# Performance work log

Measured on AMD Instinct MI355X. Metric: run time of the kernel, lower is better.

## Reference

```python
import jax, jax.numpy as jnp
import numpy as np

N_NODES = 100000
N_EDGES = 800000
D_IN = 128
D_HID = 128
N_CLASSES = 64


def _glorot(key, shape):
    fan_in, fan_out = shape[0], shape[1]
    lim = jnp.sqrt(6.0 / (fan_in + fan_out)).astype(jnp.float32)
    return jax.random.uniform(key, shape, jnp.float32, -lim, lim)


def setup_inputs() -> dict:
    key = jax.random.key(0)
    ks = jax.random.split(key, 20)
    inp = {
        "x": jax.random.normal(ks[0], (N_NODES, D_IN), jnp.float32),
        "edge_src": jax.random.randint(ks[1], (N_EDGES,), 0, N_NODES, jnp.int32),
        "edge_dst": jax.random.randint(ks[2], (N_EDGES,), 0, N_NODES, jnp.int32),
    }
    dims = [(D_IN, D_HID), (D_HID, D_HID), (D_HID, N_CLASSES)]
    k = 3
    for i, (di, do) in enumerate(dims):
        inp[f"Wp{i}"] = _glorot(ks[k], (di, di)); k += 1   # fc_pool: d_in -> d_in
        inp[f"bp{i}"] = jnp.zeros((di,), jnp.float32)
        inp[f"Ws{i}"] = _glorot(ks[k], (di, do)); k += 1   # fc_self (no bias)
        inp[f"Wn{i}"] = _glorot(ks[k], (di, do)); k += 1   # fc_neigh
        inp[f"bn{i}"] = jnp.zeros((do,), jnp.float32)
    return inp


def _sage_pool_layer(x, src, dst, Wp, bp, Ws, Wn, bn):
    # pool aggregator: max over in-edges of relu(fc_pool(h_src))
    m = jax.nn.relu(x @ Wp + bp)                 # [N, d_in]
    msg = m[src]                                 # [E, d_in] gather
    agg = jax.ops.segment_max(msg, dst, num_segments=N_NODES)  # scatter-max
    agg = jnp.where(jnp.isfinite(agg), agg, 0.0)  # zero-in-degree nodes -> 0
    return x @ Ws + agg @ Wn + bn


def reference(x, edge_src, edge_dst,
              Wp0, bp0, Ws0, Wn0, bn0,
              Wp1, bp1, Ws1, Wn1, bn1,
              Wp2, bp2, Ws2, Wn2, bn2):
    layers = [
        (Wp0, bp0, Ws0, Wn0, bn0),
        (Wp1, bp1, Ws1, Wn1, bn1),
        (Wp2, bp2, Ws2, Wn2, bn2),
    ]
    h = x
    for (Wp, bp, Ws, Wn, bn) in layers:
        # SAGEConv internal activation=relu followed by wrapper F.relu (idempotent)
        h = jax.nn.relu(_sage_pool_layer(h, edge_src, edge_dst, Wp, bp, Ws, Wn, bn))
    return jax.nn.log_softmax(h, axis=-1)
```

## Files before the change

### kernel.cpp

```cpp
#include <hip/hip_runtime.h>
#include <cstddef>
#include <cstdint>

#define NNODES 100000
#define NEDGES 800000
#define CAP 32
#define NXCD 8
#define NPB (NNODES / NXCD)
#define BINCAP 110592

typedef unsigned short u16;
typedef __attribute__((ext_vector_type(8))) short short8;
typedef __attribute__((ext_vector_type(8))) _Float16 half8;
typedef __attribute__((ext_vector_type(4))) float f32x4;
typedef __attribute__((ext_vector_type(4))) int int4v;

__device__ __forceinline__ u16 f32_to_bf16(float f) {
    union { float f; uint32_t u; } v; v.f = f;
    uint32_t r = v.u + 0x7FFF + ((v.u >> 16) & 1);
    return (u16)(r >> 16);
}
__device__ __forceinline__ u16 f32_to_f16(float f) {
    union { _Float16 h; u16 u; } v; v.h = (_Float16)f;
    return v.u;
}
__device__ __forceinline__ uint32_t pkmax(uint32_t a, uint32_t b) {
    uint32_t lo = max(a & 0xFFFFu, b & 0xFFFFu);
    uint32_t hi = max(a >> 16, b >> 16);
    return lo | (hi << 16);
}

__global__ __launch_bounds__(256) void zero_kernel(float4* __restrict__ p, int n4) {
    int i = blockIdx.x * blockDim.x + threadIdx.x;
    const int stride = gridDim.x * blockDim.x;
    for (; i < n4; i += stride) p[i] = make_float4(0.f, 0.f, 0.f, 0.f);
}

__global__ __launch_bounds__(256) void bin_kernel(
    const int* __restrict__ src, const int* __restrict__ dst,
    int* __restrict__ gcnt, int* __restrict__ bind, int* __restrict__ bins, int E)
{
    __shared__ int ld[1024], ls[1024];
    __shared__ int lcnt[8], lpre[8], lgb[8];
    const int tid = threadIdx.x;
    const int base = blockIdx.x * 1024;

    if (tid < 8) lcnt[tid] = 0;
    __syncthreads();

    int d[4], s[4], slot[4], b[4];
    int nv = 0;
    if (base + tid * 4 + 3 < E) {
        const int4v dd = *(const int4v*)&dst[base + tid * 4];
        const int4v ss = *(const int4v*)&src[base + tid * 4];
#pragma unroll
        for (int j = 0; j < 4; ++j) { d[j] = dd[j]; s[j] = ss[j]; }
        nv = 4;
    } else {
        for (int j = 0; j < 4; ++j) {
            const int idx = base + tid * 4 + j;
            if (idx < E) { d[nv] = dst[idx]; s[nv] = src[idx]; ++nv; }
        }
    }
#pragma unroll 4
    for (int j = 0; j < nv; ++j) {
        b[j] = d[j] / NPB;
        slot[j] = atomicAdd(&lcnt[b[j]], 1);
    }
    __syncthreads();
    if (tid == 0) {
        int run = 0;
#pragma unroll
        for (int k = 0; k < 8; ++k) { lpre[k] = run; run += lcnt[k]; }
    }
    __syncthreads();
#pragma unroll 4
    for (int j = 0; j < nv; ++j) {
        const int p = lpre[b[j]] + slot[j];
        ld[p] = d[j]; ls[p] = s[j];
    }
    if (tid < 8 && lcnt[tid] > 0) lgb[tid] = atomicAdd(&gcnt[tid], lcnt[tid]);
    __syncthreads();
    const int total = lpre[7] + lcnt[7];
    for (int i = tid; i < total; i += 256) {
        const int d_ = ld[i];
        const int b_ = d_ / NPB;
        const int g = lgb[b_] + (i - lpre[b_]);
        if (g < BINCAP) {
            bind[b_ * BINCAP + g] = d_;
            bins[b_ * BINCAP + g] = ls[i];
        }
    }
}

__global__ __launch_bounds__(256) void scatter_fill_kernel(
    const int* __restrict__ gcnt,
    const int* __restrict__ bind, const int* __restrict__ bins,
    int* __restrict__ deg, int* __restrict__ col2)
{
    const int xcd  = blockIdx.x & (NXCD - 1);
    const int grp  = blockIdx.x >> 3;
    const int ngrp = gridDim.x >> 3;
    int cnt = gcnt[xcd]; if (cnt > BINCAP) cnt = BINCAP;
    const int* bd = bind + xcd * BINCAP;
    const int* bs = bins + xcd * BINCAP;
    for (int i = grp * 256 + threadIdx.x; i < cnt; i += ngrp * 256) {
        const int d = bd[i];
        const int r = atomicAdd(&deg[d], 1);
        if (r < CAP) col2[d * CAP + r] = bs[i];
    }
}

struct WPtrs { const float* w[9]; };

__global__ __launch_bounds__(256) void split_weights_kernel(WPtrs p, u16* __restrict__ wbase)
{
    const int idx = blockIdx.x * 256 + threadIdx.x;
    const int w = blockIdx.y;
    const int DO_ = (w >= 7) ? 64 : 128;
    if (idx >= 128 * DO_) return;
    const float v = p.w[w][idx];
    const int k = idx / DO_;
    const int c = idx - k * DO_;
    const bool use_f16 = (w == 2 || w == 5 || w == 8);
    wbase[w * 32768 + c * 128 + k] = use_f16 ? f32_to_f16(v) : f32_to_bf16(v);
}

__global__ __launch_bounds__(256) void aggregate_kernel(
    const uint4* __restrict__ m4,
    const int* __restrict__ deg,
    const int* __restrict__ col2,
    uint4* __restrict__ agg4, int N)
{
    const int tid  = threadIdx.x;
    const int l16  = tid & 15;
    const int node = (blockIdx.x * 256 + tid) >> 4;
    if (node >= N) return;
    int cnt = deg[node];
    if (cnt > CAP) cnt = CAP;
    const int base = node * CAP;

    uint32_t a0 = 0, a1 = 0, a2 = 0, a3 = 0;
    int e = 0;
    for (; e + 4 <= cnt; e += 4) {
        const int s0 = col2[base + e],     s1 = col2[base + e + 1];
        const int s2 = col2[base + e + 2], s3 = col2[base + e + 3];
        const uint4 v0 = m4[(size_t)s0 * 16 + l16];
        const uint4 v1 = m4[(size_t)s1 * 16 + l16];
        const uint4 v2 = m4[(size_t)s2 * 16 + l16];
        const uint4 v3 = m4[(size_t)s3 * 16 + l16];
        a0 = pkmax(a0, v0.x); a1 = pkmax(a1, v0.y); a2 = pkmax(a2, v0.z); a3 = pkmax(a3, v0.w);
        a0 = pkmax(a0, v1.x); a1 = pkmax(a1, v1.y); a2 = pkmax(a2, v1.z); a3 = pkmax(a3, v1.w);
        a0 = pkmax(a0, v2.x); a1 = pkmax(a1, v2.y); a2 = pkmax(a2, v2.z); a3 = pkmax(a3, v2.w);
        a0 = pkmax(a0, v3.x); a1 = pkmax(a1, v3.y); a2 = pkmax(a2, v3.z); a3 = pkmax(a3, v3.w);
    }
    for (; e < cnt; ++e) {
        const uint4 v0 = m4[(size_t)col2[base + e] * 16 + l16];
        a0 = pkmax(a0, v0.x); a1 = pkmax(a1, v0.y); a2 = pkmax(a2, v0.z); a3 = pkmax(a3, v0.w);
    }
    agg4[(size_t)node * 16 + l16] = make_uint4(a0, a1, a2, a3);
}

template<int DO, bool DUAL, int OUT_MODE, bool AF32>
__global__ __launch_bounds__(512, 4) void mfma_gemm_kernel(
    const void* __restrict__ Av,
    const u16* __restrict__ Cq,
    const u16* __restrict__ WaT, const u16* __restrict__ WbT,
    const float* __restrict__ bias,
    float* __restrict__ outF, u16* __restrict__ outU, int N)
{
    constexpr int CT = DO / 16;
    constexpr int WS = 136;
    __shared__ u16 sW[(DUAL ? 2 : 1) * DO * WS];

    const int tid = threadIdx.x;

    for (int i = tid; i < DO * 16; i += 512) {
        const int r = i >> 4;
        const int c = (i & 15) << 3;
        *(short8*)&sW[r * WS + c] = *(const short8*)&WaT[r * 128 + c];
        if constexpr (DUAL)
            *(short8*)&sW[DO * WS + r * WS + c] = *(const short8*)&WbT[r * 128 + c];
    }

    const int lane = tid & 63;
    const int wid  = tid >> 6;
    const int l15  = lane & 15;
    const int sec  = lane >> 4;
    const int lk   = sec << 3;
    const int row0 = blockIdx.x * 128 + wid * 16;

    int aoff;
    {
        int r = row0 + l15; if (r > N - 1) r = N - 1;
        aoff = r * 128 + lk;
    }

    f32x4 acc[CT];
#pragma unroll
    for (int c = 0; c < CT; ++c) acc[c] = (f32x4){0.f, 0.f, 0.f, 0.f};

    __syncthreads();

#pragma unroll
    for (int k = 0; k < 4; ++k) {
        const int ko = 32 * k;
        short8 ah;
        if constexpr (AF32) {
            const float* pa = (const float*)Av + aoff + ko;
            f32x4 a = *(const f32x4*)pa;
            f32x4 b = *(const f32x4*)(pa + 4);
#pragma unroll
            for (int j = 0; j < 4; ++j) {
                ah[j]     = (short)f32_to_bf16(a[j]);
                ah[j + 4] = (short)f32_to_bf16(b[j]);
            }
        } else {
            ah = *(const short8*)((const u16*)Av + aoff + ko);
        }
        half8 ch;
        if constexpr (DUAL) ch = *(const half8*)(Cq + aoff + ko);
#pragma unroll
        for (int ct = 0; ct < CT; ++ct) {
            const int wb = (ct * 16 + l15) * WS + lk + ko;
            short8 wh = *(const short8*)&sW[wb];
            acc[ct] = __builtin_amdgcn_mfma_f32_16x16x32_bf16(ah, wh, acc[ct], 0, 0, 0);
            if constexpr (DUAL) {
                half8 vh = *(const half8*)&sW[DO * WS + wb];
                acc[ct] = __builtin_amdgcn_mfma_f32_16x16x32_f16(ch, vh, acc[ct], 0, 0, 0);
            }
        }
    }

    float bv[CT];
#pragma unroll
    for (int ct = 0; ct < CT; ++ct) bv[ct] = bias[ct * 16 + l15];

    const int jrow = sec << 2;
#pragma unroll
    for (int j = 0; j < 4; ++j) {
        const int r = row0 + jrow + j;
        if constexpr (OUT_MODE == 3) {
            float v[CT];
            float mx = 0.f;
#pragma unroll
            for (int ct = 0; ct < CT; ++ct) {
                v[ct] = fmaxf(acc[ct][j] + bv[ct], 0.f);
                mx = fmaxf(mx, v[ct]);
            }
#pragma unroll
            for (int off = 1; off < 16; off <<= 1) mx = fmaxf(mx, __shfl_xor(mx, off));
            float s = 0.f;
#pragma unroll
            for (int ct = 0; ct < CT; ++ct) s += __expf(v[ct] - mx);
#pragma unroll
            for (int off = 1; off < 16; off <<= 1) s += __shfl_xor(s, off);
            const float lse = mx + __logf(s);
            if (r < N) {
#pragma unroll
                for (int ct = 0; ct < CT; ++ct)
                    outF[(size_t)r * DO + ct * 16 + l15] = v[ct] - lse;
            }
        } else if (r < N) {
#pragma unroll
            for (int ct = 0; ct < CT; ++ct) {
                float v = fmaxf(acc[ct][j] + bv[ct], 0.f);
                const size_t o = (size_t)r * DO + ct * 16 + l15;
                if constexpr (OUT_MODE == 1) {
                    outU[o] = f32_to_bf16(v);
                } else {
                    outU[o] = f32_to_f16(v);
                }
            }
        }
    }
}

extern "C" void kernel_launch(void* const* d_in, const int* in_sizes, int n_in,
                              void* d_out, int out_size, void* d_ws, size_t ws_size,
                              hipStream_t stream)
{
    const int N = NNODES, E = NEDGES;
    const float* x  = (const float*)d_in[0];
    const int* esrc = (const int*)d_in[1];
    const int* edst = (const int*)d_in[2];
    const float* bp[3] = {(const float*)d_in[4], (const float*)d_in[9],  (const float*)d_in[14]};
    const float* bn[3] = {(const float*)d_in[7], (const float*)d_in[12], (const float*)d_in[17]};

    char* ws = (char*)d_ws;
    const size_t P = (size_t)N * 128 * 2;
    u16* p0 = (u16*)(ws);
    char* p1 = ws + P;
    u16* p2 = (u16*)(ws + 2 * P);
    char* p3 = ws + 3 * P;
    u16* p4 = (u16*)(ws + 4 * P);
    u16* p5 = (u16*)(ws + 5 * P);
    u16* wbase = (u16*)(p3 + 2 * 8 * BINCAP * 4 + 4096);

    int* deg  = (int*)p1;
    int* gcnt = (int*)(p1 + 400000);
    int* col2 = (int*)(p1 + 409600);
    int* bind = (int*)p3;
    int* bins = bind + 8 * BINCAP;
    auto WT = [&](int i) { return wbase + i * 32768; };

    const int gg = (N + 127) / 128;
    const int ablocks = (N * 16 + 255) / 256;
    const int bblocks = (E + 1023) / 1024;
    dim3 blk(256), gblk(512);

    zero_kernel<<<128, blk, 0, stream>>>((float4*)p1, 409600 / 16);
    bin_kernel<<<bblocks, blk, 0, stream>>>(esrc, edst, gcnt, bind, bins, E);
    scatter_fill_kernel<<<2048, blk, 0, stream>>>(gcnt, bind, bins, deg, col2);

    WPtrs wp;
    wp.w[0] = (const float*)d_in[3];  wp.w[1] = (const float*)d_in[5];  wp.w[2] = (const float*)d_in[6];
    wp.w[3] = (const float*)d_in[8];  wp.w[4] = (const float*)d_in[10]; wp.w[5] = (const float*)d_in[11];
    wp.w[6] = (const float*)d_in[13]; wp.w[7] = (const float*)d_in[15]; wp.w[8] = (const float*)d_in[16];
    split_weights_kernel<<<dim3(64, 9), blk, 0, stream>>>(wp, wbase);

    mfma_gemm_kernel<128, false, 2, true><<<gg, gblk, 0, stream>>>(
        x, nullptr, WT(0), nullptr, bp[0], nullptr, p4, N);
    aggregate_kernel<<<ablocks, blk, 0, stream>>>((const uint4*)p4, deg, col2, (uint4*)p5, N);
    mfma_gemm_kernel<128, true, 1, true><<<gg, gblk, 0, stream>>>(
        x, p5, WT(1), WT(2), bn[0], nullptr, p2, N);

    mfma_gemm_kernel<128, false, 2, false><<<gg, gblk, 0, stream>>>(
        p2, nullptr, WT(3), nullptr, bp[1], nullptr, p4, N);
    aggregate_kernel<<<ablocks, blk, 0, stream>>>((const uint4*)p4, deg, col2, (uint4*)p5, N);
    mfma_gemm_kernel<128, true, 1, false><<<gg, gblk, 0, stream>>>(
        p2, p5, WT(4), WT(5), bn[1], nullptr, p0, N);

    mfma_gemm_kernel<128, false, 2, false><<<gg, gblk, 0, stream>>>(
        p0, nullptr, WT(6), nullptr, bp[2], nullptr, p4, N);
    aggregate_kernel<<<ablocks, blk, 0, stream>>>((const uint4*)p4, deg, col2, (uint4*)p5, N);
    mfma_gemm_kernel<64, true, 3, false><<<gg, gblk, 0, stream>>>(
        p0, p5, WT(7), WT(8), bn[2], (float*)d_out, nullptr, N);
}
```

Baseline: 272.1 us.

## Sort nodes by in-degree for aggregation and pre-cast input to bf16

Adds a counting sort of nodes by clamped in-degree (histogram, scan, fill kernels) so the aggregate kernel runs nodes in degree order, which reduces wavefront divergence from uneven neighbour counts. The node id and its count are packed into one int. The fp32 input x is also cast to bf16 once by a separate kernel, so the first two GEMMs read bf16 instead of converting fp32 inline. The cost is four extra launches, an extra pass over x, and scattered output writes in aggregation.

Result: slower. 286.6 us (+5.3%).

```diff
diff --git a/kernel.cpp b/kernel.cpp
--- a/kernel.cpp
+++ b/kernel.cpp
@@ -111,6 +111,60 @@
     }
 }
 
+__global__ __launch_bounds__(256) void sort_hist_kernel(
+    const int* __restrict__ deg, int* __restrict__ hist, int N)
+{
+    __shared__ int lh[33];
+    const int t = threadIdx.x;
+    if (t < 33) lh[t] = 0;
+    __syncthreads();
+    const int n = blockIdx.x * 256 + t;
+    if (n < N) atomicAdd(&lh[min(deg[n], CAP)], 1);
+    __syncthreads();
+    if (t < 33 && lh[t]) atomicAdd(&hist[t], lh[t]);
+}
+
+__global__ __launch_bounds__(64) void sort_scan_kernel(int* __restrict__ hist)
+{
+    if (threadIdx.x == 0) {
+        int run = 0;
+        for (int b = 0; b < 33; ++b) { const int c = hist[b]; hist[b] = run; run += c; }
+    }
+}
+
+__global__ __launch_bounds__(256) void sort_fill_kernel(
+    const int* __restrict__ deg, int* __restrict__ binptr,
+    int* __restrict__ order, int N)
+{
+    __shared__ int lh[33], lgb[33];
+    const int t = threadIdx.x;
+    if (t < 33) lh[t] = 0;
+    __syncthreads();
+    const int n = blockIdx.x * 256 + t;
+    int b = 0, slot = 0;
+    if (n < N) {
+        b = min(deg[n], CAP);
+        slot = atomicAdd(&lh[b], 1);
+    }
+    __syncthreads();
+    if (t < 33 && lh[t]) lgb[t] = atomicAdd(&binptr[t], lh[t]);
+    __syncthreads();
+    if (n < N) order[lgb[b] + slot] = n | (b << 20);
+}
+
+__global__ __launch_bounds__(256) void bf16_cast_kernel(
+    const float4* __restrict__ in, uint2* __restrict__ out, int n4)
+{
+    int i = blockIdx.x * 256 + threadIdx.x;
+    const int stride = gridDim.x * 256;
+    for (; i < n4; i += stride) {
+        float4 v = in[i];
+        out[i] = make_uint2(
+            (uint32_t)f32_to_bf16(v.x) | ((uint32_t)f32_to_bf16(v.y) << 16),
+            (uint32_t)f32_to_bf16(v.z) | ((uint32_t)f32_to_bf16(v.w) << 16));
+    }
+}
+
 struct WPtrs { const float* w[9]; };
 
 __global__ __launch_bounds__(256) void split_weights_kernel(WPtrs p, u16* __restrict__ wbase)
@@ -128,16 +182,17 @@
 
 __global__ __launch_bounds__(256) void aggregate_kernel(
     const uint4* __restrict__ m4,
-    const int* __restrict__ deg,
+    const int* __restrict__ order,
     const int* __restrict__ col2,
     uint4* __restrict__ agg4, int N)
 {
     const int tid  = threadIdx.x;
     const int l16  = tid & 15;
-    const int node = (blockIdx.x * 256 + tid) >> 4;
-    if (node >= N) return;
-    int cnt = deg[node];
-    if (cnt > CAP) cnt = CAP;
+    const int idx  = (blockIdx.x * 256 + tid) >> 4;
+    if (idx >= N) return;
+    const int oe   = order[idx];
+    const int node = oe & 0xFFFFF;
+    const int cnt  = oe >> 20;
     const int base = node * CAP;
 
     uint32_t a0 = 0, a1 = 0, a2 = 0, a3 = 0;
@@ -161,9 +216,9 @@
     agg4[(size_t)node * 16 + l16] = make_uint4(a0, a1, a2, a3);
 }
 
-template<int DO, bool DUAL, int OUT_MODE, bool AF32>
+template<int DO, bool DUAL, int OUT_MODE>
 __global__ __launch_bounds__(512, 4) void mfma_gemm_kernel(
-    const void* __restrict__ Av,
+    const u16* __restrict__ A,
     const u16* __restrict__ Cq,
     const u16* __restrict__ WaT, const u16* __restrict__ WbT,
     const float* __restrict__ bias,
@@ -205,19 +260,7 @@
 #pragma unroll
     for (int k = 0; k < 4; ++k) {
         const int ko = 32 * k;
-        short8 ah;
-        if constexpr (AF32) {
-            const float* pa = (const float*)Av + aoff + ko;
-            f32x4 a = *(const f32x4*)pa;
-            f32x4 b = *(const f32x4*)(pa + 4);
-#pragma unroll
-            for (int j = 0; j < 4; ++j) {
-                ah[j]     = (short)f32_to_bf16(a[j]);
-                ah[j + 4] = (short)f32_to_bf16(b[j]);
-            }
-        } else {
-            ah = *(const short8*)((const u16*)Av + aoff + ko);
-        }
+        short8 ah = *(const short8*)(A + aoff + ko);
         half8 ch;
         if constexpr (DUAL) ch = *(const half8*)(Cq + aoff + ko);
 #pragma unroll
@@ -295,45 +338,53 @@
     char* p3 = ws + 3 * P;
     u16* p4 = (u16*)(ws + 4 * P);
     u16* p5 = (u16*)(ws + 5 * P);
-    u16* wbase = (u16*)(p3 + 2 * 8 * BINCAP * 4 + 4096);
-
-    int* deg  = (int*)p1;
-    int* gcnt = (int*)(p1 + 400000);
-    int* col2 = (int*)(p1 + 409600);
-    int* bind = (int*)p3;
-    int* bins = bind + 8 * BINCAP;
+
+    int* deg    = (int*)p1;
+    int* gcnt   = (int*)(p1 + 400000);
+    int* hist   = (int*)(p1 + 400064);
+    int* binptr = (int*)(p1 + 400256);
+    int* col2   = (int*)(p1 + 409600);
+    int* bind   = (int*)p3;
+    int* bins   = bind + 8 * BINCAP;
+    int* order  = bins + 8 * BINCAP;
+    u16* wbase  = (u16*)(order + NNODES + 64);
     auto WT = [&](int i) { return wbase + i * 32768; };
 
     const int gg = (N + 127) / 128;
     const int ablocks = (N * 16 + 255) / 256;
     const int bblocks = (E + 1023) / 1024;
+    const int nblocks = (N + 255) / 256;
     dim3 blk(256), gblk(512);
 
     zero_kernel<<<128, blk, 0, stream>>>((float4*)p1, 409600 / 16);
     bin_kernel<<<bblocks, blk, 0, stream>>>(esrc, edst, gcnt, bind, bins, E);
     scatter_fill_kernel<<<2048, blk, 0, stream>>>(gcnt, bind, bins, deg, col2);
+    sort_hist_kernel<<<nblocks, blk, 0, stream>>>(deg, hist, N);
+    sort_scan_kernel<<<1, 64, 0, stream>>>(hist);
+    sort_fill_kernel<<<nblocks, blk, 0, stream>>>(deg, hist, order, N);
 
     WPtrs wp;
     wp.w[0] = (const float*)d_in[3];  wp.w[1] = (const float*)d_in[5];  wp.w[2] = (const float*)d_in[6];
     wp.w[3] = (const float*)d_in[8];  wp.w[4] = (const float*)d_in[10]; wp.w[5] = (const float*)d_in[11];
     wp.w[6] = (const float*)d_in[13]; wp.w[7] = (const float*)d_in[15]; wp.w[8] = (const float*)d_in[16];
     split_weights_kernel<<<dim3(64, 9), blk, 0, stream>>>(wp, wbase);
-
-    mfma_gemm_kernel<128, false, 2, true><<<gg, gblk, 0, stream>>>(
-        x, nullptr, WT(0), nullptr, bp[0], nullptr, p4, N);
-    aggregate_kernel<<<ablocks, blk, 0, stream>>>((const uint4*)p4, deg, col2, (uint4*)p5, N);
-    mfma_gemm_kernel<128, true, 1, true><<<gg, gblk, 0, stream>>>(
-        x, p5, WT(1), WT(2), bn[0], nullptr, p2, N);
-
-    mfma_gemm_kernel<128, false, 2, false><<<gg, gblk, 0, stream>>>(
+    bf16_cast_kernel<<<2048, blk, 0, stream>>>((const float4*)x, (uint2*)p0, N * 128 / 4);
+
+    mfma_gemm_kernel<128, false, 2><<<gg, gblk, 0, stream>>>(
+        p0, nullptr, WT(0), nullptr, bp[0], nullptr, p4, N);
+    aggregate_kernel<<<ablocks, blk, 0, stream>>>((const uint4*)p4, order, col2, (uint4*)p5, N);
+    mfma_gemm_kernel<128, true, 1><<<gg, gblk, 0, stream>>>(
+        p0, p5, WT(1), WT(2), bn[0], nullptr, p2, N);
+
+    mfma_gemm_kernel<128, false, 2><<<gg, gblk, 0, stream>>>(
         p2, nullptr, WT(3), nullptr, bp[1], nullptr, p4, N);
-    aggregate_kernel<<<ablocks, blk, 0, stream>>>((const uint4*)p4, deg, col2, (uint4*)p5, N);
-    mfma_gemm_kernel<128, true, 1, false><<<gg, gblk, 0, stream>>>(
+    aggregate_kernel<<<ablocks, blk, 0, stream>>>((const uint4*)p4, order, col2, (uint4*)p5, N);
+    mfma_gemm_kernel<128, true, 1><<<gg, gblk, 0, stream>>>(
         p2, p5, WT(4), WT(5), bn[1], nullptr, p0, N);
 
-    mfma_gemm_kernel<128, false, 2, false><<<gg, gblk, 0, stream>>>(
+    mfma_gemm_kernel<128, false, 2><<<gg, gblk, 0, stream>>>(
         p0, nullptr, WT(6), nullptr, bp[2], nullptr, p4, N);
-    aggregate_kernel<<<ablocks, blk, 0, stream>>>((const uint4*)p4, deg, col2, (uint4*)p5, N);
-    mfma_gemm_kernel<64, true, 3, false><<<gg, gblk, 0, stream>>>(
+    aggregate_kernel<<<ablocks, blk, 0, stream>>>((const uint4*)p4, order, col2, (uint4*)p5, N);
+    mfma_gemm_kernel<64, true, 3><<<gg, gblk, 0, stream>>>(
         p0, p5, WT(7), WT(8), bn[2], (float*)d_out, nullptr, N);
 }
```
